# Kernel tuning notes

Measured on AMD Instinct MI355X. Metric: run time of the kernel, lower is better.

The kernel has to match this reference:

```python
import jax, jax.numpy as jnp
import numpy as np

NUM_HEADS = 6

def setup_inputs() -> dict:
    key = jax.random.key(0)
    k1, k2, k3 = jax.random.split(key, 3)
    B, N, C = 8, 4096, 768
    x = jax.random.normal(k1, (B, N, C), dtype=jnp.float32)
    # torch Linear weights, stored here as (in, out) so y = x @ w
    w_qkv = jax.random.normal(k2, (C, 3 * C), dtype=jnp.float32) * (C ** -0.5)
    w_proj = jax.random.normal(k3, (C, C), dtype=jnp.float32) * (C ** -0.5)
    b_proj = jnp.zeros((C,), dtype=jnp.float32)
    return {"x": x, "w_qkv": w_qkv, "w_proj": w_proj, "b_proj": b_proj}

def reference(x, w_qkv, w_proj, b_proj):
    B, N, C = x.shape
    H = NUM_HEADS
    D = C // H
    scale = D ** -0.5
    qkv = (x @ w_qkv).reshape(B, N, 3, H, D)
    q, k, v = qkv[:, :, 0], qkv[:, :, 1], qkv[:, :, 2]  # each (B, N, H, D)
    # NOTE: faithful to source — no permute, so attention is over the HEAD axis
    attn = jnp.einsum('bnhd,bngd->bnhg', q, k) * scale  # (B, N, H, H)
    attn = jax.nn.softmax(attn, axis=-1)
    out = jnp.einsum('bnhg,bngd->bnhd', attn, v)        # (B, N, H, D)
    # torch: .transpose(1,2).reshape(B, N, C) — replicate the exact dim mixing
    out = jnp.transpose(out, (0, 2, 1, 3)).reshape(B, N, C)
    return out @ w_proj + b_proj
```

## Files before the change

kernel.cpp:

```cpp
#include <hip/hip_runtime.h>
#include <hip/hip_bf16.h>
#include <stdint.h>

typedef __attribute__((ext_vector_type(8))) short short8;
typedef __attribute__((ext_vector_type(4))) float floatx4;

#define DEVINL static __device__ __forceinline__

DEVINL float bf2f(uint32_t u) {
  union { uint32_t i; float f; } x; x.i = u << 16; return x.f;
}
DEVINL float bfu(short v) {
  union { uint32_t i; float f; } x; x.i = ((uint32_t)(uint16_t)v) << 16; return x.f;
}
DEVINL uint16_t f2bf(float f) {
  union { float f; uint32_t i; } x; x.f = f;
  uint32_t i = x.i;
  i += 0x7fff + ((i >> 16) & 1);
  return (uint16_t)(i >> 16);
}

__global__ __launch_bounds__(256)
void k_cvt_bf16(const float* __restrict__ in, uint16_t* __restrict__ out, int n4) {
  int i = blockIdx.x * blockDim.x + threadIdx.x;
  int stride = gridDim.x * blockDim.x;
  for (; i < n4; i += stride) {
    float4 v = ((const float4*)in)[i];
    ushort4 o;
    o.x = f2bf(v.x); o.y = f2bf(v.y); o.z = f2bf(v.z); o.w = f2bf(v.w);
    ((ushort4*)out)[i] = o;
  }
}

__global__ __launch_bounds__(256)
void k_transpose_bf16(const float* __restrict__ in, uint16_t* __restrict__ out, int K, int N) {
  __shared__ float tile[64][65];
  const int tn = blockIdx.x * 64;
  const int tk = blockIdx.y * 64;
  const int tx = threadIdx.x & 63;
  const int ty = threadIdx.x >> 6;
#pragma unroll
  for (int i = 0; i < 64; i += 4)
    tile[ty + i][tx] = in[(long)(tk + ty + i) * N + tn + tx];
  __syncthreads();
#pragma unroll
  for (int i = 0; i < 64; i += 4)
    out[(long)(tn + ty + i) * K + tk + tx] = f2bf(tile[tx][ty + i]);
}

template<int OUT_BF16>
__global__ __launch_bounds__(512, 2)
void k_gemm256(const uint16_t* __restrict__ A,
               const uint16_t* __restrict__ B,
               void* __restrict__ Cout,
               const float* __restrict__ bias,
               int M, int N, int Kd, int tilesN)
{
  __shared__ uint16_t As[2][2][8192];
  __shared__ uint16_t Bs[2][2][8192];

  const int nwg = gridDim.x;
  const int orig = blockIdx.x;
  const int q = nwg >> 3, r = nwg & 7;
  const int xcd = orig & 7, seq = orig >> 3;
  const int wgid = (xcd < r ? xcd * (q + 1) : r * (q + 1) + (xcd - r) * q) + seq;
  const int mt = wgid / tilesN;
  const int nt = wgid - mt * tilesN;

  const int t = threadIdx.x;
  const int l = t & 63;
  const int w = t >> 6;
  const int wm = w >> 2;
  const int wn = w & 3;
  const long m0 = (long)mt * 256;
  const long n0 = (long)nt * 256;

  const int srow0 = t >> 3;
  const int scol  = ((l & 7) ^ (l >> 3)) * 8;
  const int wbyte = w * 1024;

  const uint16_t* Abase = A + m0 * Kd;
  const uint16_t* Bbase = B + n0 * Kd;

  const int fr = l & 15;
  const int kg = l >> 4;
  const int xorv = (l & 7) << 4;
  const int cb0 = (kg * 16) ^ xorv;
  const int cb1 = (64 + kg * 16) ^ xorv;

  floatx4 acc[8][4];
#pragma unroll
  for (int m = 0; m < 8; ++m)
#pragma unroll
    for (int n = 0; n < 4; ++n)
      acc[m][n] = (floatx4){0.f, 0.f, 0.f, 0.f};

  const int nK = Kd >> 6;

  auto stage = [&](uint16_t* ldsHalf, const uint16_t* gHalf, int ktile) {
    const uint16_t* g0 = gHalf + (long)srow0 * Kd + ktile * 64 + scol;
    __builtin_amdgcn_global_load_lds(
        (const __attribute__((address_space(1))) void*)g0,
        (__attribute__((address_space(3))) void*)((char*)ldsHalf + wbyte), 16, 0, 0);
    __builtin_amdgcn_global_load_lds(
        (const __attribute__((address_space(1))) void*)(g0 + (long)64 * Kd),
        (__attribute__((address_space(3))) void*)((char*)ldsHalf + 8192 + wbyte), 16, 0, 0);
  };
  auto rdA = [&](int buf, int mm, int kk) -> short8 {
    const char* p = (const char*)&As[buf][wm][0] + mm * 2048 + fr * 128 + (kk ? cb1 : cb0);
    return *(const short8*)p;
  };
  auto rdB = [&](int buf, int nn, int kk) -> short8 {
    const char* p = (const char*)&Bs[buf][wn >> 1][0] + (wn & 1) * 8192 + nn * 2048 + fr * 128
                    + (kk ? cb1 : cb0);
    return *(const short8*)p;
  };

  stage(&Bs[0][0][0], Bbase, 0);
  stage(&Bs[0][1][0], Bbase + (long)128 * Kd, 0);
  stage(&As[0][0][0], Abase, 0);
  stage(&As[0][1][0], Abase + (long)128 * Kd, 0);
  {
    int t1 = 1 % nK;
    stage(&Bs[t1 & 1][0][0], Bbase, t1);
    stage(&As[t1 & 1][0][0], Abase, t1);
  }
  asm volatile("s_waitcnt vmcnt(4)" ::: "memory");
  __builtin_amdgcn_s_barrier();

  short8 a[4][2], a2[4][2], bv0[2][2], bv1[2][2];

  for (int kt = 0; kt < nK; ++kt) {
    const int cbuf = kt & 1;
    const int nbuf = cbuf ^ 1;
    const int t1 = (kt + 1) % nK;
    const int t2 = (kt + 2) % nK;

    stage(&Bs[nbuf][1][0], Bbase + (long)128 * Kd, t1);
    stage(&As[nbuf][1][0], Abase + (long)128 * Kd, t1);

#pragma unroll
    for (int mm = 0; mm < 4; ++mm) { a[mm][0] = rdA(cbuf, mm, 0); a[mm][1] = rdA(cbuf, mm, 1); }
#pragma unroll
    for (int nn = 0; nn < 2; ++nn) { bv0[nn][0] = rdB(cbuf, nn, 0); bv0[nn][1] = rdB(cbuf, nn, 1); }
#pragma unroll
    for (int nn = 0; nn < 2; ++nn) { bv1[nn][0] = rdB(cbuf, 2 + nn, 0); bv1[nn][1] = rdB(cbuf, 2 + nn, 1); }
#pragma unroll
    for (int mm = 0; mm < 4; ++mm) { a2[mm][0] = rdA(cbuf, 4 + mm, 0); a2[mm][1] = rdA(cbuf, 4 + mm, 1); }

    asm volatile("s_waitcnt lgkmcnt(8)" ::: "memory");
    __builtin_amdgcn_s_setprio(1);
#pragma unroll
    for (int mm = 0; mm < 4; ++mm)
#pragma unroll
      for (int nn = 0; nn < 2; ++nn) {
        acc[mm][nn] = __builtin_amdgcn_mfma_f32_16x16x32_bf16(a[mm][0], bv0[nn][0], acc[mm][nn], 0, 0, 0);
        acc[mm][nn] = __builtin_amdgcn_mfma_f32_16x16x32_bf16(a[mm][1], bv0[nn][1], acc[mm][nn], 0, 0, 0);
        acc[mm][2 + nn] = __builtin_amdgcn_mfma_f32_16x16x32_bf16(a[mm][0], bv1[nn][0], acc[mm][2 + nn], 0, 0, 0);
        acc[mm][2 + nn] = __builtin_amdgcn_mfma_f32_16x16x32_bf16(a[mm][1], bv1[nn][1], acc[mm][2 + nn], 0, 0, 0);
      }
    asm volatile("s_waitcnt lgkmcnt(0)" ::: "memory");
    __builtin_amdgcn_s_barrier();

    stage(&Bs[cbuf][0][0], Bbase, t2);
    stage(&As[cbuf][0][0], Abase, t2);
#pragma unroll
    for (int mm = 0; mm < 4; ++mm)
#pragma unroll
      for (int nn = 0; nn < 2; ++nn) {
        acc[4 + mm][nn] = __builtin_amdgcn_mfma_f32_16x16x32_bf16(a2[mm][0], bv0[nn][0], acc[4 + mm][nn], 0, 0, 0);
        acc[4 + mm][nn] = __builtin_amdgcn_mfma_f32_16x16x32_bf16(a2[mm][1], bv0[nn][1], acc[4 + mm][nn], 0, 0, 0);
        acc[4 + mm][2 + nn] = __builtin_amdgcn_mfma_f32_16x16x32_bf16(a2[mm][0], bv1[nn][0], acc[4 + mm][2 + nn], 0, 0, 0);
        acc[4 + mm][2 + nn] = __builtin_amdgcn_mfma_f32_16x16x32_bf16(a2[mm][1], bv1[nn][1], acc[4 + mm][2 + nn], 0, 0, 0);
      }
    __builtin_amdgcn_s_setprio(0);

    asm volatile("s_waitcnt vmcnt(4)" ::: "memory");
    __builtin_amdgcn_s_barrier();
  }

  asm volatile("s_waitcnt vmcnt(0)" ::: "memory");
  __builtin_amdgcn_s_barrier();

  const int orow = (l >> 4) * 4;
  const int ocol = l & 15;
  if (OUT_BF16) {
    uint16_t* C = (uint16_t*)Cout;
    char* eb = (char*)&As[0][0][0] + (size_t)w * 4096;
    const int rr0 = l >> 3;
    const int cc0 = (l & 7) * 8;
#pragma unroll
    for (int mm = 0; mm < 8; ++mm) {
#pragma unroll
      for (int nn = 0; nn < 4; ++nn)
#pragma unroll
        for (int r2 = 0; r2 < 4; ++r2) {
          int rrow = orow + r2;
          int byo = ((rrow * 64 + nn * 16 + ocol) * 2) ^ ((rrow & 7) << 4);
          *(uint16_t*)(eb + byo) = f2bf(acc[mm][nn][r2]);
        }
#pragma unroll
      for (int p = 0; p < 2; ++p) {
        int rrow = rr0 + p * 8;
        int byo = ((rrow * 64 + cc0) * 2) ^ ((rrow & 7) << 4);
        short8 vvv = *(const short8*)(eb + byo);
        *(short8*)(&C[(m0 + wm * 128 + mm * 16 + rrow) * N + n0 + wn * 64 + cc0]) = vvv;
      }
    }
  } else {
    float* C = (float*)Cout;
    float* eb = (float*)&As[0][0][0] + (size_t)w * 1024;
    const int rr0 = l >> 4;
    const int cc0 = (l & 15) * 4;
    float4 bias4 = make_float4(0.f, 0.f, 0.f, 0.f);
    if (bias) bias4 = *(const float4*)(bias + n0 + wn * 64 + cc0);
#pragma unroll
    for (int mm = 0; mm < 8; ++mm) {
#pragma unroll
      for (int nn = 0; nn < 4; ++nn)
#pragma unroll
        for (int r2 = 0; r2 < 4; ++r2)
          eb[(orow + r2) * 64 + nn * 16 + ocol] = acc[mm][nn][r2];
#pragma unroll
      for (int p = 0; p < 4; ++p) {
        int rrow = rr0 + p * 4;
        float4 vvv = *(const float4*)(eb + rrow * 64 + cc0);
        vvv.x += bias4.x; vvv.y += bias4.y; vvv.z += bias4.z; vvv.w += bias4.w;
        *(float4*)(&C[(m0 + wm * 128 + mm * 16 + rrow) * N + n0 + wn * 64 + cc0]) = vvv;
      }
    }
  }
}

__global__ __launch_bounds__(256)
void k_attn(const uint16_t* __restrict__ qkv, uint16_t* __restrict__ outp) {
  const int wid = blockIdx.x * 4 + (threadIdx.x >> 6);
  const int l = threadIdx.x & 63;
  const int sub = l >> 4;
  const int i = l & 15;
  const int token = wid * 4 + sub;
  const uint16_t* row = qkv + (long)token * 2304 + i * 8;

  short8 kv[6];
  float qf[6][8];
#pragma unroll
  for (int h = 0; h < 6; ++h) {
    short8 qv = *(const short8*)(row + h * 128);
    kv[h] = *(const short8*)(row + 768 + h * 128);
#pragma unroll
    for (int e = 0; e < 8; ++e) qf[h][e] = bfu(qv[e]);
  }

  float s[36];
#pragma unroll
  for (int g = 0; g < 6; ++g) {
    float kf[8];
#pragma unroll
    for (int e = 0; e < 8; ++e) kf[e] = bfu(kv[g][e]);
#pragma unroll
    for (int h = 0; h < 6; ++h) {
      float a = 0.f;
#pragma unroll
      for (int e = 0; e < 8; ++e) a += qf[h][e] * kf[e];
      s[h * 6 + g] = a;
    }
  }

#pragma unroll
  for (int off = 8; off > 0; off >>= 1)
#pragma unroll
    for (int j = 0; j < 36; ++j)
      s[j] += __shfl_xor(s[j], off, 64);

  const float scale = 0.088388347648318447f;
  float p[36];
#pragma unroll
  for (int h = 0; h < 6; ++h) {
    float mx = s[h * 6];
#pragma unroll
    for (int g = 1; g < 6; ++g) mx = fmaxf(mx, s[h * 6 + g]);
    float sum = 0.f;
#pragma unroll
    for (int g = 0; g < 6; ++g) {
      float e = __expf((s[h * 6 + g] - mx) * scale);
      p[h * 6 + g] = e; sum += e;
    }
    float inv = 1.f / sum;
#pragma unroll
    for (int g = 0; g < 6; ++g) p[h * 6 + g] *= inv;
  }

  float o[6][8];
#pragma unroll
  for (int h = 0; h < 6; ++h)
#pragma unroll
    for (int e = 0; e < 8; ++e) o[h][e] = 0.f;
#pragma unroll
  for (int g = 0; g < 6; ++g) {
    short8 vv = *(const short8*)(row + 1536 + g * 128);
    float vf[8];
#pragma unroll
    for (int e = 0; e < 8; ++e) vf[e] = bfu(vv[e]);
#pragma unroll
    for (int h = 0; h < 6; ++h)
#pragma unroll
      for (int e = 0; e < 8; ++e) o[h][e] += p[h * 6 + g] * vf[e];
  }

  const int b = token >> 12, nn = token & 4095;
#pragma unroll
  for (int h = 0; h < 6; ++h) {
    short8 ov;
#pragma unroll
    for (int e = 0; e < 8; ++e) ov[e] = (short)f2bf(o[h][e]);
    *(short8*)(outp + ((long)(b * 6 + h) * 4096 + nn) * 128 + i * 8) = ov;
  }
}

extern "C" void kernel_launch(void* const* d_in, const int* in_sizes, int n_in,
                              void* d_out, int out_size, void* d_ws, size_t ws_size,
                              hipStream_t stream) {
  const float* x      = (const float*)d_in[0];
  const float* w_qkv  = (const float*)d_in[1];
  const float* w_proj = (const float*)d_in[2];
  const float* b_proj = (const float*)d_in[3];
  float* out = (float*)d_out;

  const int Cc = 768, C3 = 2304;
  const int Mtok = in_sizes[0] / Cc;

  char* ws = (char*)d_ws;
  uint16_t* x_bf   = (uint16_t*)ws;
  uint16_t* att_bf = x_bf;
  uint16_t* qkv_bf = (uint16_t*)(ws + 50331648);
  uint16_t* wqkvT  = (uint16_t*)(ws + 50331648 + 150994944);
  uint16_t* wprojT = (uint16_t*)(ws + 50331648 + 150994944 + 3538944);

  hipLaunchKernelGGL(k_cvt_bf16, dim3(2048), dim3(256), 0, stream,
                     x, x_bf, Mtok * Cc / 4);
  hipLaunchKernelGGL(k_transpose_bf16, dim3(C3 / 64, Cc / 64), dim3(256), 0, stream,
                     w_qkv, wqkvT, Cc, C3);
  hipLaunchKernelGGL(k_transpose_bf16, dim3(Cc / 64, Cc / 64), dim3(256), 0, stream,
                     w_proj, wprojT, Cc, Cc);

  hipLaunchKernelGGL((k_gemm256<1>), dim3((Mtok / 256) * (C3 / 256)), dim3(512), 0, stream,
                     x_bf, wqkvT, (void*)qkv_bf, (const float*)nullptr, Mtok, C3, Cc, C3 / 256);

  hipLaunchKernelGGL(k_attn, dim3(Mtok / 16), dim3(256), 0, stream, qkv_bf, att_bf);

  hipLaunchKernelGGL((k_gemm256<0>), dim3((Mtok / 256) * (Cc / 256)), dim3(512), 0, stream,
                     att_bf, wprojT, (void*)out, b_proj, Mtok, Cc, Cc, Cc / 256);
}
```

Before: 275.8 us.

## Fuse fp32-to-bf16 conversion of x into the QKV GEMM A-tile loads

Drops the separate conversion kernel for x. A new QKV GEMM loads fp32 x tiles straight into registers, converts them with packed bf16 converts and writes them into LDS, while B tiles keep using direct global-to-LDS loads. This avoids writing and then re-reading a 48MB bf16 copy of x. In exchange, each workgroup reads fp32 A data, which doubles A traffic and is repeated across the 9 N-tiles, and the register staging adds VGPR pressure. The LDS fragment reads in the existing GEMM are also moved ahead of the next-tile staging.

```diff
diff --git a/kernel.cpp b/kernel.cpp
--- a/kernel.cpp
+++ b/kernel.cpp
@@ -7,9 +7,6 @@
 
 #define DEVINL static __device__ __forceinline__
 
-DEVINL float bf2f(uint32_t u) {
-  union { uint32_t i; float f; } x; x.i = u << 16; return x.f;
-}
 DEVINL float bfu(short v) {
   union { uint32_t i; float f; } x; x.i = ((uint32_t)(uint16_t)v) << 16; return x.f;
 }
@@ -19,17 +16,10 @@
   i += 0x7fff + ((i >> 16) & 1);
   return (uint16_t)(i >> 16);
 }
-
-__global__ __launch_bounds__(256)
-void k_cvt_bf16(const float* __restrict__ in, uint16_t* __restrict__ out, int n4) {
-  int i = blockIdx.x * blockDim.x + threadIdx.x;
-  int stride = gridDim.x * blockDim.x;
-  for (; i < n4; i += stride) {
-    float4 v = ((const float4*)in)[i];
-    ushort4 o;
-    o.x = f2bf(v.x); o.y = f2bf(v.y); o.z = f2bf(v.z); o.w = f2bf(v.w);
-    ((ushort4*)out)[i] = o;
-  }
+DEVINL uint32_t cvtpk(float lo, float hi) {
+  uint32_t r;
+  asm("v_cvt_pk_bf16_f32 %0, %1, %2" : "=v"(r) : "v"(lo), "v"(hi));
+  return r;
 }
 
 __global__ __launch_bounds__(256)
@@ -46,6 +36,188 @@
 #pragma unroll
   for (int i = 0; i < 64; i += 4)
     out[(long)(tn + ty + i) * K + tk + tx] = f2bf(tile[tx][ty + i]);
+}
+
+__global__ __launch_bounds__(512, 2)
+void k_gemm1f(const float* __restrict__ X,
+              const uint16_t* __restrict__ B,
+              uint16_t* __restrict__ Cout,
+              int M, int N, int Kd, int tilesN)
+{
+  __shared__ uint16_t As[2][2][8192];
+  __shared__ uint16_t Bs[2][2][8192];
+
+  const int nwg = gridDim.x;
+  const int orig = blockIdx.x;
+  const int q = nwg >> 3, r = nwg & 7;
+  const int xcd = orig & 7, seq = orig >> 3;
+  const int wgid = (xcd < r ? xcd * (q + 1) : r * (q + 1) + (xcd - r) * q) + seq;
+  const int mt = wgid / tilesN;
+  const int nt = wgid - mt * tilesN;
+
+  const int t = threadIdx.x;
+  const int l = t & 63;
+  const int w = t >> 6;
+  const int wm = w >> 2;
+  const int wn = w & 3;
+  const long m0 = (long)mt * 256;
+  const long n0 = (long)nt * 256;
+
+  const int srow0 = t >> 3;
+  const int scol  = ((l & 7) ^ (l >> 3)) * 8;
+  const int wbyte = w * 1024;
+
+  const float* Xbase = X + m0 * Kd;
+  const uint16_t* Bbase = B + n0 * Kd;
+
+  const int fr = l & 15;
+  const int kg = l >> 4;
+  const int xorv = (l & 7) << 4;
+  const int cb0 = (kg * 16) ^ xorv;
+  const int cb1 = (64 + kg * 16) ^ xorv;
+
+  floatx4 acc[8][4];
+#pragma unroll
+  for (int m = 0; m < 8; ++m)
+#pragma unroll
+    for (int n = 0; n < 4; ++n)
+      acc[m][n] = (floatx4){0.f, 0.f, 0.f, 0.f};
+
+  const int nK = Kd >> 6;
+
+  auto stageB = [&](uint16_t* ldsHalf, const uint16_t* gHalf, int ktile) {
+    const uint16_t* g0 = gHalf + (long)srow0 * Kd + ktile * 64 + scol;
+    __builtin_amdgcn_global_load_lds(
+        (const __attribute__((address_space(1))) void*)g0,
+        (__attribute__((address_space(3))) void*)((char*)ldsHalf + wbyte), 16, 0, 0);
+    __builtin_amdgcn_global_load_lds(
+        (const __attribute__((address_space(1))) void*)(g0 + (long)64 * Kd),
+        (__attribute__((address_space(3))) void*)((char*)ldsHalf + 8192 + wbyte), 16, 0, 0);
+  };
+  auto loadA = [&](int ktile, float4* fa) {
+    const float* g = Xbase + (long)srow0 * Kd + ktile * 64 + scol;
+#pragma unroll
+    for (int p = 0; p < 4; ++p) {
+      fa[2 * p]     = *(const float4*)(g + (long)64 * p * Kd);
+      fa[2 * p + 1] = *(const float4*)(g + (long)64 * p * Kd + 4);
+    }
+  };
+  auto writeA = [&](int buf, const float4* fa) {
+    char* base = (char*)&As[buf][0][0];
+#pragma unroll
+    for (int p = 0; p < 4; ++p) {
+      uint4 pk;
+      pk.x = cvtpk(fa[2 * p].x, fa[2 * p].y);
+      pk.y = cvtpk(fa[2 * p].z, fa[2 * p].w);
+      pk.z = cvtpk(fa[2 * p + 1].x, fa[2 * p + 1].y);
+      pk.w = cvtpk(fa[2 * p + 1].z, fa[2 * p + 1].w);
+      *(uint4*)(base + (p >> 1) * 16384 + (p & 1) * 8192 + wbyte + l * 16) = pk;
+    }
+  };
+  auto rdA = [&](int buf, int mm, int kk) -> short8 {
+    const char* p = (const char*)&As[buf][wm][0] + mm * 2048 + fr * 128 + (kk ? cb1 : cb0);
+    return *(const short8*)p;
+  };
+  auto rdB = [&](int buf, int nn, int kk) -> short8 {
+    const char* p = (const char*)&Bs[buf][wn >> 1][0] + (wn & 1) * 8192 + nn * 2048 + fr * 128
+                    + (kk ? cb1 : cb0);
+    return *(const short8*)p;
+  };
+
+  stageB(&Bs[0][0][0], Bbase, 0);
+  stageB(&Bs[0][1][0], Bbase + (long)128 * Kd, 0);
+  {
+    float4 fa[8];
+    loadA(0, fa);
+    int t1 = 1 % nK;
+    stageB(&Bs[t1 & 1][0][0], Bbase, t1);
+    asm volatile("s_waitcnt vmcnt(2)" ::: "memory");
+    writeA(0, fa);
+    asm volatile("s_waitcnt lgkmcnt(0)" ::: "memory");
+  }
+  __builtin_amdgcn_s_barrier();
+
+  short8 a[4][2], a2[4][2], bv0[2][2], bv1[2][2];
+
+  for (int kt = 0; kt < nK; ++kt) {
+    const int cbuf = kt & 1;
+    const int nbuf = cbuf ^ 1;
+    const int t1 = (kt + 1) % nK;
+    const int t2 = (kt + 2) % nK;
+
+#pragma unroll
+    for (int mm = 0; mm < 4; ++mm) { a[mm][0] = rdA(cbuf, mm, 0); a[mm][1] = rdA(cbuf, mm, 1); }
+#pragma unroll
+    for (int nn = 0; nn < 2; ++nn) { bv0[nn][0] = rdB(cbuf, nn, 0); bv0[nn][1] = rdB(cbuf, nn, 1); }
+#pragma unroll
+    for (int nn = 0; nn < 2; ++nn) { bv1[nn][0] = rdB(cbuf, 2 + nn, 0); bv1[nn][1] = rdB(cbuf, 2 + nn, 1); }
+#pragma unroll
+    for (int mm = 0; mm < 4; ++mm) { a2[mm][0] = rdA(cbuf, 4 + mm, 0); a2[mm][1] = rdA(cbuf, 4 + mm, 1); }
+
+    stageB(&Bs[nbuf][1][0], Bbase + (long)128 * Kd, t1);
+    float4 fa[8];
+    loadA(t1, fa);
+
+    asm volatile("s_waitcnt lgkmcnt(8)" ::: "memory");
+    __builtin_amdgcn_s_setprio(1);
+#pragma unroll
+    for (int mm = 0; mm < 4; ++mm)
+#pragma unroll
+      for (int nn = 0; nn < 2; ++nn) {
+        acc[mm][nn] = __builtin_amdgcn_mfma_f32_16x16x32_bf16(a[mm][0], bv0[nn][0], acc[mm][nn], 0, 0, 0);
+        acc[mm][nn] = __builtin_amdgcn_mfma_f32_16x16x32_bf16(a[mm][1], bv0[nn][1], acc[mm][nn], 0, 0, 0);
+        acc[mm][2 + nn] = __builtin_amdgcn_mfma_f32_16x16x32_bf16(a[mm][0], bv1[nn][0], acc[mm][2 + nn], 0, 0, 0);
+        acc[mm][2 + nn] = __builtin_amdgcn_mfma_f32_16x16x32_bf16(a[mm][1], bv1[nn][1], acc[mm][2 + nn], 0, 0, 0);
+      }
+    asm volatile("s_waitcnt lgkmcnt(0)" ::: "memory");
+    __builtin_amdgcn_s_barrier();
+
+    stageB(&Bs[cbuf][0][0], Bbase, t2);
+#pragma unroll
+    for (int mm = 0; mm < 4; ++mm)
+#pragma unroll
+      for (int nn = 0; nn < 2; ++nn) {
+        acc[4 + mm][nn] = __builtin_amdgcn_mfma_f32_16x16x32_bf16(a2[mm][0], bv0[nn][0], acc[4 + mm][nn], 0, 0, 0);
+        acc[4 + mm][nn] = __builtin_amdgcn_mfma_f32_16x16x32_bf16(a2[mm][1], bv0[nn][1], acc[4 + mm][nn], 0, 0, 0);
+        acc[4 + mm][2 + nn] = __builtin_amdgcn_mfma_f32_16x16x32_bf16(a2[mm][0], bv1[nn][0], acc[4 + mm][2 + nn], 0, 0, 0);
+        acc[4 + mm][2 + nn] = __builtin_amdgcn_mfma_f32_16x16x32_bf16(a2[mm][1], bv1[nn][1], acc[4 + mm][2 + nn], 0, 0, 0);
+      }
+    __builtin_amdgcn_s_setprio(0);
+
+    asm volatile("s_waitcnt vmcnt(2)" ::: "memory");
+    writeA(nbuf, fa);
+    asm volatile("s_waitcnt lgkmcnt(0)" ::: "memory");
+    __builtin_amdgcn_s_barrier();
+  }
+
+  asm volatile("s_waitcnt vmcnt(0)" ::: "memory");
+  __builtin_amdgcn_s_barrier();
+
+  const int orow = (l >> 4) * 4;
+  const int ocol = l & 15;
+  {
+    char* eb = (char*)&As[0][0][0] + (size_t)w * 4096;
+    const int rr0 = l >> 3;
+    const int cc0 = (l & 7) * 8;
+#pragma unroll
+    for (int mm = 0; mm < 8; ++mm) {
+#pragma unroll
+      for (int nn = 0; nn < 4; ++nn)
+#pragma unroll
+        for (int r2 = 0; r2 < 4; ++r2) {
+          int rrow = orow + r2;
+          int byo = ((rrow * 64 + nn * 16 + ocol) * 2) ^ ((rrow & 7) << 4);
+          *(uint16_t*)(eb + byo) = f2bf(acc[mm][nn][r2]);
+        }
+#pragma unroll
+      for (int p = 0; p < 2; ++p) {
+        int rrow = rr0 + p * 8;
+        int byo = ((rrow * 64 + cc0) * 2) ^ ((rrow & 7) << 4);
+        short8 vvv = *(const short8*)(eb + byo);
+        *(short8*)(&Cout[(m0 + wm * 128 + mm * 16 + rrow) * N + n0 + wn * 64 + cc0]) = vvv;
+      }
+    }
+  }
 }
 
 template<int OUT_BF16>
@@ -136,17 +308,17 @@
     const int t1 = (kt + 1) % nK;
     const int t2 = (kt + 2) % nK;
 
+#pragma unroll
+    for (int mm = 0; mm < 4; ++mm) { a[mm][0] = rdA(cbuf, mm, 0); a[mm][1] = rdA(cbuf, mm, 1); }
+#pragma unroll
+    for (int nn = 0; nn < 2; ++nn) { bv0[nn][0] = rdB(cbuf, nn, 0); bv0[nn][1] = rdB(cbuf, nn, 1); }
+#pragma unroll
+    for (int nn = 0; nn < 2; ++nn) { bv1[nn][0] = rdB(cbuf, 2 + nn, 0); bv1[nn][1] = rdB(cbuf, 2 + nn, 1); }
+#pragma unroll
+    for (int mm = 0; mm < 4; ++mm) { a2[mm][0] = rdA(cbuf, 4 + mm, 0); a2[mm][1] = rdA(cbuf, 4 + mm, 1); }
+
     stage(&Bs[nbuf][1][0], Bbase + (long)128 * Kd, t1);
     stage(&As[nbuf][1][0], Abase + (long)128 * Kd, t1);
-
-#pragma unroll
-    for (int mm = 0; mm < 4; ++mm) { a[mm][0] = rdA(cbuf, mm, 0); a[mm][1] = rdA(cbuf, mm, 1); }
-#pragma unroll
-    for (int nn = 0; nn < 2; ++nn) { bv0[nn][0] = rdB(cbuf, nn, 0); bv0[nn][1] = rdB(cbuf, nn, 1); }
-#pragma unroll
-    for (int nn = 0; nn < 2; ++nn) { bv1[nn][0] = rdB(cbuf, 2 + nn, 0); bv1[nn][1] = rdB(cbuf, 2 + nn, 1); }
-#pragma unroll
-    for (int mm = 0; mm < 4; ++mm) { a2[mm][0] = rdA(cbuf, 4 + mm, 0); a2[mm][1] = rdA(cbuf, 4 + mm, 1); }
 
     asm volatile("s_waitcnt lgkmcnt(8)" ::: "memory");
     __builtin_amdgcn_s_setprio(1);
@@ -330,21 +502,18 @@
   const int Mtok = in_sizes[0] / Cc;
 
   char* ws = (char*)d_ws;
-  uint16_t* x_bf   = (uint16_t*)ws;
-  uint16_t* att_bf = x_bf;
+  uint16_t* att_bf = (uint16_t*)ws;
   uint16_t* qkv_bf = (uint16_t*)(ws + 50331648);
   uint16_t* wqkvT  = (uint16_t*)(ws + 50331648 + 150994944);
   uint16_t* wprojT = (uint16_t*)(ws + 50331648 + 150994944 + 3538944);
 
-  hipLaunchKernelGGL(k_cvt_bf16, dim3(2048), dim3(256), 0, stream,
-                     x, x_bf, Mtok * Cc / 4);
   hipLaunchKernelGGL(k_transpose_bf16, dim3(C3 / 64, Cc / 64), dim3(256), 0, stream,
                      w_qkv, wqkvT, Cc, C3);
   hipLaunchKernelGGL(k_transpose_bf16, dim3(Cc / 64, Cc / 64), dim3(256), 0, stream,
                      w_proj, wprojT, Cc, Cc);
 
-  hipLaunchKernelGGL((k_gemm256<1>), dim3((Mtok / 256) * (C3 / 256)), dim3(512), 0, stream,
-                     x_bf, wqkvT, (void*)qkv_bf, (const float*)nullptr, Mtok, C3, Cc, C3 / 256);
+  hipLaunchKernelGGL(k_gemm1f, dim3((Mtok / 256) * (C3 / 256)), dim3(512), 0, stream,
+                     x, wqkvT, qkv_bf, Mtok, C3, Cc, C3 / 256);
 
   hipLaunchKernelGGL(k_attn, dim3(Mtok / 16), dim3(256), 0, stream, qkv_bf, att_bf);
 
```

Measured after the change: 350.0 us. 26.9% more time.
